# Kernel optimization log

Hardware: AMD Instinct MI355X
Metric: run time of the kernel (lower is better)

## Reference

```python
import jax, jax.numpy as jnp
import numpy as np

T = 0.07  # temperature from init default


def _l2norm(x):
    return x / jnp.linalg.norm(x, axis=1, keepdims=True)


def setup_inputs() -> dict:
    key = jax.random.key(0)
    ks = jax.random.split(key, 12)
    B, D, K = 512, 128, 4096
    G = M = 131072
    return {
        "feat": jax.random.normal(ks[0], (B, D), jnp.float32),
        "label": jax.random.randint(ks[1], (B,), 0, 2),
        "out": jnp.zeros((B, K + 1), jnp.float32),   # unused by forward
        "name": jnp.arange(B),                        # unused by forward
        "y": jax.random.randint(ks[2], (B,), 0, G),   # unused by forward
        "memory_feat_gbm": jax.random.normal(ks[3], (G, D), jnp.float32),
        "memory_prob_gbm": jax.random.uniform(ks[4], (G,), jnp.float32),
        "memory_feat_mate": jax.random.normal(ks[5], (M, D), jnp.float32),
        "memory_prob_mate": jax.random.uniform(ks[6], (M,), jnp.float32),
        "idx_n_g": jax.random.randint(ks[7], (K, 1), 0, G),
        "idx_p_g": jax.random.randint(ks[8], (1, 1), 0, G // 4),
        "idx_n_m": jax.random.randint(ks[9], (K, 1), 0, M),
        "idx_p_m": jax.random.randint(ks[10], (1, 1), 0, M // 4),
    }


def reference(feat, label, out, name, y, memory_feat_gbm, memory_prob_gbm,
              memory_feat_mate, memory_prob_mate, idx_n_g, idx_p_g, idx_n_m, idx_p_m):
    # __init__ normalizes the memory banks once
    mfg = _l2norm(memory_feat_gbm)
    mfm = _l2norm(memory_feat_mate)
    feat_n = _l2norm(feat)  # [B, D]
    output_size = mfg.shape[0]

    # gather positive / negative prototypes (all rows unit-norm, so
    # cosine_similarity == dot product)
    wp_g = mfg[idx_p_g.ravel()]   # [1, D]
    wn_g = mfg[idx_n_g.ravel()]   # [K, D]
    wp_m = mfm[idx_p_m.ravel()]   # [1, D]
    wn_m = mfm[idx_n_m.ravel()]   # [K, D]

    # label==0 (gbm): pos from gbm bank, negs from mate bank; label==1 mirrored
    row_gbm = jnp.concatenate([feat_n @ wp_g.T, feat_n @ wn_m.T], axis=1)   # [B, K+1]
    row_mate = jnp.concatenate([feat_n @ wp_m.T, feat_n @ wn_g.T], axis=1)  # [B, K+1]
    sims = jnp.where((label == 0)[:, None], row_gbm, row_mate)

    # use_softmax=False path: exp(s/T) / Z with Z set from first batch (treated as constant)
    e = jnp.exp(sims / T)
    Z = jax.lax.stop_gradient(e.mean() * output_size)
    out_feature_p_n = e / Z

    # confident cluster members + current batch (data-dependent sizes; eager jax)
    mask_g = memory_prob_gbm > 0.5
    mask_m = memory_prob_mate > 0.6
    feature_clu_all = jnp.concatenate([mfg[mask_g], mfm[mask_m], feat_n], axis=0)
    gt_clu_all = jnp.concatenate([
        jnp.zeros((int(mask_g.sum()),), label.dtype),
        jnp.ones((int(mask_m.sum()),), label.dtype),
        label,
    ], axis=0)
    return out_feature_p_n, feature_clu_all, gt_clu_all
```

## Files before the change

kernel.cpp:

```cpp
#include <hip/hip_runtime.h>
#include <math.h>


#define TINV 14.2857142857142857f
#define JT 64
#define BT 32

__device__ __forceinline__ float wredsum64(float v) {
#pragma unroll
  for (int m = 32; m > 0; m >>= 1) v += __shfl_xor(v, m, 64);
  return v;
}

__global__ __launch_bounds__(256) void k_stageA(
    const float* __restrict__ feat, const int* __restrict__ label,
    const float* __restrict__ mfg, const float* __restrict__ pg,
    const float* __restrict__ mfm, const float* __restrict__ pm,
    const int* __restrict__ idxpg, const int* __restrict__ idxpm,
    float* __restrict__ outp, long long cluTail, long long gtTail,
    int* __restrict__ bucket, int* __restrict__ n0p,
    int* __restrict__ cg, int* __restrict__ cm,
    float* __restrict__ posPartials,
    int B, int K1, int G, int M,
    int nCountBlk, int nFeatBlk, int nPosBlk) {
  int bid = blockIdx.x, t = threadIdx.x;

  if (bid < nCountBlk) {
    __shared__ int s[8];
    int i = bid * 256 + t;
    int a = (i < G) && (pg[i] > 0.5f);
    int b = (i < M) && (pm[i] > 0.6f);
    unsigned long long ba = __ballot(a), bb = __ballot(b);
    int lane = t & 63, w = t >> 6;
    if (lane == 0) { s[w] = __popcll(ba); s[4 + w] = __popcll(bb); }
    __syncthreads();
    if (t == 0) cg[bid] = s[0] + s[1] + s[2] + s[3];
    if (t == 1) cm[bid] = s[4] + s[5] + s[6] + s[7];
    return;
  }
  bid -= nCountBlk;

  if (bid < nFeatBlk) {
    int gid = bid * 256 + t;
    int w = gid >> 6, lane = gid & 63;
    if (w < B) {
      float2 v = ((const float2*)feat)[(long long)w * 64 + lane];
      float sq = wredsum64(v.x * v.x + v.y * v.y);
      float inv = rsqrtf(sq);
      ((float2*)(outp + cluTail))[(long long)w * 64 + lane] =
          make_float2(v.x * inv, v.y * inv);
      if (lane == 0) outp[gtTail + w] = (float)label[w];
    }
    return;
  }
  bid -= nFeatBlk;

  if (bid < nPosBlk) {
    __shared__ float ps[4];
    int gid = bid * 256 + t;
    int w = gid >> 6, lane = gid & 63, lw = t >> 6;
    float e = 0.f;
    if (w < B) {
      int lab = label[w];
      const float* bank = lab ? mfm : mfg;
      long long row = lab ? idxpm[0] : idxpg[0];
      float2 wv = ((const float2*)(bank + row * 128))[lane];
      float2 fv = ((const float2*)feat)[(long long)w * 64 + lane];
      float dot = wredsum64(fv.x * wv.x + fv.y * wv.y);
      float sqw = wredsum64(wv.x * wv.x + wv.y * wv.y);
      float sqf = wredsum64(fv.x * fv.x + fv.y * fv.y);
      e = expf(dot * rsqrtf(sqw) * rsqrtf(sqf) * TINV);
      if (lane == 0) outp[(long long)w * K1] = e;
    }
    if (lane == 0) ps[lw] = e;
    __syncthreads();
    if (t == 0) posPartials[bid] = ps[0] + ps[1] + ps[2] + ps[3];
    return;
  }

  {
    __shared__ int sc[512];
    int t2 = t + 256;
    int m0 = (t < B) ? (label[t] == 0 ? 1 : 0) : 0;
    int m1 = (t2 < B) ? (label[t2] == 0 ? 1 : 0) : 0;
    sc[t] = m0; sc[t2] = m1;
    __syncthreads();
    for (int off = 1; off < 512; off <<= 1) {
      int u0 = (t >= off) ? sc[t - off] : 0;
      int u1 = (t2 >= off) ? sc[t2 - off] : 0;
      __syncthreads();
      sc[t] += u0; sc[t2] += u1;
      __syncthreads();
    }
    int n0 = (B > 0) ? sc[B - 1] : 0;
    if (t < B) {
      int incl = sc[t];
      if (m0) bucket[incl - 1] = t; else bucket[n0 + t - incl] = t;
    }
    if (t2 < B) {
      int incl = sc[t2];
      if (m1) bucket[incl - 1] = t2; else bucket[n0 + t2 - incl] = t2;
    }
    if (t == 0) *n0p = n0;
  }
}

__global__ __launch_bounds__(256) void k_stageB(
    const float* __restrict__ featn, const int* __restrict__ bucket,
    const int* __restrict__ n0ptr,
    const float* __restrict__ mfg, const float* __restrict__ mfm,
    const float* __restrict__ pg, const float* __restrict__ pm,
    const int* __restrict__ idxng, const int* __restrict__ idxnm,
    const int* __restrict__ cg, const int* __restrict__ cm,
    float* __restrict__ out0, float* __restrict__ partials,
    float* __restrict__ outp, long long cluBase, long long gtBase,
    int B, int K, int K1, int G, int M, int NB, int simsGx, int nGatherBlk) {
  int t = threadIdx.x;

  if ((int)blockIdx.x < nGatherBlk) {
    int bid = blockIdx.x;
    int bankId = bid / NB;
    int cb = bid - bankId * NB;
    const float* probs = bankId ? pm : pg;
    const float* rows  = bankId ? mfm : mfg;
    float thr = bankId ? 0.6f : 0.5f;
    int Nelem = bankId ? M : G;
    int lane = t & 63, w = t >> 6;

    int j0 = t, j1 = t + 256;
    int s = 0;
    if (bankId == 0) {
      if (j0 < cb) s += cg[j0];
      if (j1 < cb && j1 < NB) s += cg[j1];
    } else {
      if (j0 < NB) s += cg[j0];
      if (j1 < NB) s += cg[j1];
      if (j0 < cb) s += cm[j0];
      if (j1 < cb && j1 < NB) s += cm[j1];
    }
#pragma unroll
    for (int m = 32; m > 0; m >>= 1) s += __shfl_xor(s, m, 64);

    __shared__ int red[4];
    __shared__ int woff[4];
    __shared__ int selRow[256];
    if (lane == 0) red[w] = s;

    int i = cb * 256 + t;
    int f = (i < Nelem) && (probs[i] > thr);
    unsigned long long mball = __ballot(f);
    if (lane == 0) woff[w] = __popcll(mball);
    __syncthreads();

    long long off = (long long)red[0] + red[1] + red[2] + red[3];
    int pre = 0;
#pragma unroll
    for (int q = 0; q < 3; q++)
      if (q < w) pre += woff[q];
    int S = woff[0] + woff[1] + woff[2] + woff[3];
    unsigned long long below = lane ? ((~0ull) >> (64 - lane)) : 0ull;
    if (f) selRow[pre + __popcll(mball & below)] = i;
    __syncthreads();

    float labv = (float)bankId;
    int hw = t >> 5, l = t & 31;
    for (int r = hw; r < S; r += 8) {
      long long src = selRow[r];
      float4 v = ((const float4*)(rows + src * 128))[l];
      float sq = v.x * v.x + v.y * v.y + v.z * v.z + v.w * v.w;
#pragma unroll
      for (int m = 16; m > 0; m >>= 1) sq += __shfl_xor(sq, m, 64);
      float inv = rsqrtf(sq);
      long long dst = off + r;
      ((float4*)(outp + cluBase + dst * 128))[l] =
          make_float4(v.x * inv, v.y * inv, v.z * inv, v.w * inv);
      if (l == 0) outp[gtBase + dst] = labv;
    }
    return;
  }

  __shared__ float4 wl[JT][33];
  __shared__ float4 fl[BT][33];
  __shared__ float invw[JT];
  __shared__ float bs[4];
  int pidx = (int)blockIdx.x - nGatherBlk;
  int bx = pidx % simsGx, by = pidx / simsGx;
  int n0 = *n0ptr;
  int nb0 = (n0 + BT - 1) / BT;
  int lab, p0, cnt;
  if (by < nb0) {
    lab = 0; p0 = by * BT; cnt = min(BT, n0 - p0);
  } else {
    int k = by - nb0; p0 = n0 + k * BT;
    int n1 = B - n0; cnt = min(BT, n1 - k * BT); lab = 1;
  }
  if (cnt <= 0) { if (t == 0) partials[pidx] = 0.f; return; }
  const float* bank = lab == 0 ? mfm : mfg;
  const int* idxN   = lab == 0 ? idxnm : idxng;
  int j0 = bx * JT;

#pragma unroll
  for (int q = 0; q < 8; q++) {
    int lin = q * 256 + t;
    int row = lin >> 5, col = lin & 31;
    long long srow = idxN[j0 + row];
    wl[row][col] = ((const float4*)(bank + srow * 128))[col];
  }
#pragma unroll
  for (int q = 0; q < 4; q++) {
    int lin = q * 256 + t;
    int row = lin >> 5, col = lin & 31;
    float4 v = make_float4(0.f, 0.f, 0.f, 0.f);
    if (row < cnt) {
      int bg = bucket[p0 + row];
      v = ((const float4*)(featn + (long long)bg * 128))[col];
    }
    fl[row][col] = v;
  }
  __syncthreads();

  {
    int r = t >> 2, q = t & 3;
    float ss = 0.f;
#pragma unroll
    for (int c = 0; c < 8; c++) {
      float4 v = wl[r][q * 8 + c];
      ss += v.x * v.x + v.y * v.y + v.z * v.z + v.w * v.w;
    }
    ss += __shfl_xor(ss, 1, 64);
    ss += __shfl_xor(ss, 2, 64);
    if (q == 0) invw[r] = rsqrtf(ss);
  }
  __syncthreads();

  int tj = t & 15, tb = t >> 4;
  float acc[4][2];
#pragma unroll
  for (int a = 0; a < 4; a++)
#pragma unroll
    for (int b = 0; b < 2; b++) acc[a][b] = 0.f;

#pragma unroll 4
  for (int i = 0; i < 32; i++) {
    float4 w0 = wl[tj][i];
    float4 w1 = wl[tj + 16][i];
    float4 w2 = wl[tj + 32][i];
    float4 w3 = wl[tj + 48][i];
    float4 f0 = fl[tb][i];
    float4 f1 = fl[tb + 16][i];
    acc[0][0] += w0.x*f0.x + w0.y*f0.y + w0.z*f0.z + w0.w*f0.w;
    acc[1][0] += w1.x*f0.x + w1.y*f0.y + w1.z*f0.z + w1.w*f0.w;
    acc[2][0] += w2.x*f0.x + w2.y*f0.y + w2.z*f0.z + w2.w*f0.w;
    acc[3][0] += w3.x*f0.x + w3.y*f0.y + w3.z*f0.z + w3.w*f0.w;
    acc[0][1] += w0.x*f1.x + w0.y*f1.y + w0.z*f1.z + w0.w*f1.w;
    acc[1][1] += w1.x*f1.x + w1.y*f1.y + w1.z*f1.z + w1.w*f1.w;
    acc[2][1] += w2.x*f1.x + w2.y*f1.y + w2.z*f1.z + w2.w*f1.w;
    acc[3][1] += w3.x*f1.x + w3.y*f1.y + w3.z*f1.z + w3.w*f1.w;
  }

  float mysum = 0.f;
#pragma unroll
  for (int bb = 0; bb < 2; bb++) {
    int bl = tb + 16 * bb;
    if (bl < cnt) {
      int bg = bucket[p0 + bl];
#pragma unroll
      for (int jj = 0; jj < 4; jj++) {
        int jr = tj + 16 * jj;
        float e = expf(acc[jj][bb] * invw[jr] * TINV);
        out0[(long long)bg * K1 + 1 + j0 + jr] = e;
        mysum += e;
      }
    }
  }
  float wsum = wredsum64(mysum);
  if ((t & 63) == 0) bs[t >> 6] = wsum;
  __syncthreads();
  if (t == 0) partials[pidx] = bs[0] + bs[1] + bs[2] + bs[3];
}

__global__ __launch_bounds__(256) void k_stageD(
    float* __restrict__ out0, const float* __restrict__ partials, int nPart,
    double factor, long long n4) {
  __shared__ double sd[256];
  int t = threadIdx.x;
  double s = 0.0;
  for (int i = t; i < nPart; i += 256) s += (double)partials[i];
  sd[t] = s;
  __syncthreads();
  for (int off = 128; off > 0; off >>= 1) {
    if (t < off) sd[t] += sd[t + off];
    __syncthreads();
  }
  float sc = (float)(factor / sd[0]);
  long long base = (long long)blockIdx.x * 256 + t;
  long long stride = (long long)gridDim.x * 256;
  for (long long i = base; i < n4; i += stride) {
    float4 v = ((float4*)out0)[i];
    v.x *= sc; v.y *= sc; v.z *= sc; v.w *= sc;
    ((float4*)out0)[i] = v;
  }
}

extern "C" void kernel_launch(void* const* d_in, const int* in_sizes, int n_in,
                              void* d_out, int out_size, void* d_ws,
                              size_t ws_size, hipStream_t stream) {
  const float* feat  = (const float*)d_in[0];
  const int*   label = (const int*)d_in[1];
  const float* mfg   = (const float*)d_in[5];
  const float* pg    = (const float*)d_in[6];
  const float* mfm   = (const float*)d_in[7];
  const float* pm    = (const float*)d_in[8];
  const int*   idxng = (const int*)d_in[9];
  const int*   idxpg = (const int*)d_in[10];
  const int*   idxnm = (const int*)d_in[11];
  const int*   idxpm = (const int*)d_in[12];
  float* outp = (float*)d_out;

  const int B = in_sizes[1];
  const int D = 128;
  const int K = in_sizes[9];
  const int G = in_sizes[6];
  const int M = in_sizes[8];
  const int K1 = K + 1;

  const long long C0 = (long long)B * K1;
  const long long R = ((long long)out_size - C0) / (D + 1);
  const long long G0 = C0 + R * D;
  const long long cluTail = C0 + (R - B) * (long long)D;
  const long long gtTail = G0 + (R - B);

  const float* featn = outp + cluTail;

  char* wsb = (char*)d_ws;
  size_t o = 0;
  auto alloc = [&](size_t bytes) -> char* {
    char* p = wsb + o;
    o = (o + bytes + 255) & ~(size_t)255;
    return p;
  };
  const int simsGx = K / JT;
  const int simsGy = B / BT + 1;
  const int nPartSims = simsGx * simsGy;
  const int nPosBlk = (B * 64 + 255) / 256;
  float* partials = (float*)alloc(sizeof(float) * (nPartSims + nPosBlk));
  int* bucket = (int*)alloc(sizeof(int) * B);
  int* n0p = (int*)alloc(sizeof(int) * 4);
  const int NB = ((G > M ? G : M) + 255) / 256;
  int* cg = (int*)alloc(sizeof(int) * NB);
  int* cm = (int*)alloc(sizeof(int) * NB);
  (void)ws_size; (void)n_in;

  const int nFeatBlk = (B * 64 + 255) / 256;
  const int gridA = NB + nFeatBlk + nPosBlk + 1;
  const int nGatherBlk = 2 * NB;
  const int gridB = nGatherBlk + nPartSims;
  const int gridD = 2048;

  k_stageA<<<gridA, 256, 0, stream>>>(
      feat, label, mfg, pg, mfm, pm, idxpg, idxpm,
      outp, cluTail, gtTail, bucket, n0p, cg, cm,
      partials + nPartSims, B, K1, G, M, NB, nFeatBlk, nPosBlk);

  k_stageB<<<gridB, 256, 0, stream>>>(
      featn, bucket, n0p, mfg, mfm, pg, pm, idxng, idxnm,
      cg, cm, outp, partials, outp, C0, G0,
      B, K, K1, G, M, NB, simsGx, nGatherBlk);

  double factor = (double)B * (double)K1 / (double)G;
  k_stageD<<<gridD, 256, 0, stream>>>(
      outp, partials, nPartSims + nPosBlk, factor, C0 / 4);
}
```

Measured before the change: 52.15 us.

## Refine compaction gather to 64-row chunks and schedule sims blocks first

Stage A now records per-wavefront mask counts in 64-element granularity instead of per 256-element block, which drops a shared-memory barrier. Stage B's gather blocks each handle 64 candidate rows, so there are four times as many blocks but each is shorter. Each half-wave now processes two rows per iteration for more memory-level parallelism, and blocks with no selected rows exit early. The sims tiles are moved to the front of the grid so the heavier GEMM-like blocks start first. In exchange, every gather block scans a prefix array four times longer and more blocks are launched.

```diff
diff --git a/kernel.cpp b/kernel.cpp
--- a/kernel.cpp
+++ b/kernel.cpp
@@ -19,23 +19,22 @@
     const int* __restrict__ idxpg, const int* __restrict__ idxpm,
     float* __restrict__ outp, long long cluTail, long long gtTail,
     int* __restrict__ bucket, int* __restrict__ n0p,
-    int* __restrict__ cg, int* __restrict__ cm,
+    int* __restrict__ cg64, int* __restrict__ cm64,
     float* __restrict__ posPartials,
     int B, int K1, int G, int M,
     int nCountBlk, int nFeatBlk, int nPosBlk) {
   int bid = blockIdx.x, t = threadIdx.x;
 
   if (bid < nCountBlk) {
-    __shared__ int s[8];
     int i = bid * 256 + t;
     int a = (i < G) && (pg[i] > 0.5f);
     int b = (i < M) && (pm[i] > 0.6f);
     unsigned long long ba = __ballot(a), bb = __ballot(b);
     int lane = t & 63, w = t >> 6;
-    if (lane == 0) { s[w] = __popcll(ba); s[4 + w] = __popcll(bb); }
-    __syncthreads();
-    if (t == 0) cg[bid] = s[0] + s[1] + s[2] + s[3];
-    if (t == 1) cm[bid] = s[4] + s[5] + s[6] + s[7];
+    if (lane == 0) {
+      cg64[bid * 4 + w] = __popcll(ba);
+      cm64[bid * 4 + w] = __popcll(bb);
+    }
     return;
   }
   bid -= nCountBlk;
@@ -111,70 +110,77 @@
     const float* __restrict__ mfg, const float* __restrict__ mfm,
     const float* __restrict__ pg, const float* __restrict__ pm,
     const int* __restrict__ idxng, const int* __restrict__ idxnm,
-    const int* __restrict__ cg, const int* __restrict__ cm,
+    const int* __restrict__ cg64, const int* __restrict__ cm64,
     float* __restrict__ out0, float* __restrict__ partials,
     float* __restrict__ outp, long long cluBase, long long gtBase,
-    int B, int K, int K1, int G, int M, int NB, int simsGx, int nGatherBlk) {
+    int B, int K, int K1, int G, int M, int NG64, int simsGx, int nSimsBlk) {
   int t = threadIdx.x;
 
-  if ((int)blockIdx.x < nGatherBlk) {
-    int bid = blockIdx.x;
-    int bankId = bid / NB;
-    int cb = bid - bankId * NB;
+  if ((int)blockIdx.x >= nSimsBlk) {
+    int gb = (int)blockIdx.x - nSimsBlk;
+    int bankId = gb / NG64;
+    int g = gb - bankId * NG64;
     const float* probs = bankId ? pm : pg;
     const float* rows  = bankId ? mfm : mfg;
     float thr = bankId ? 0.6f : 0.5f;
     int Nelem = bankId ? M : G;
     int lane = t & 63, w = t >> 6;
 
-    int j0 = t, j1 = t + 256;
     int s = 0;
-    if (bankId == 0) {
-      if (j0 < cb) s += cg[j0];
-      if (j1 < cb && j1 < NB) s += cg[j1];
-    } else {
-      if (j0 < NB) s += cg[j0];
-      if (j1 < NB) s += cg[j1];
-      if (j0 < cb) s += cm[j0];
-      if (j1 < cb && j1 < NB) s += cm[j1];
+    for (int j = t; j < NG64; j += 256) {
+      if (bankId == 0) {
+        if (j < g) s += cg64[j];
+      } else {
+        s += cg64[j];
+        if (j < g) s += cm64[j];
+      }
     }
 #pragma unroll
     for (int m = 32; m > 0; m >>= 1) s += __shfl_xor(s, m, 64);
 
     __shared__ int red[4];
-    __shared__ int woff[4];
-    __shared__ int selRow[256];
+    __shared__ int selRow[64];
     if (lane == 0) red[w] = s;
 
-    int i = cb * 256 + t;
-    int f = (i < Nelem) && (probs[i] > thr);
-    unsigned long long mball = __ballot(f);
-    if (lane == 0) woff[w] = __popcll(mball);
+    int c = g * 64 + lane;
+    int f = (c < Nelem) && (probs[c] > thr);
+    unsigned long long mb = __ballot(f);
+    if (w == 0) {
+      unsigned long long below = lane ? ((~0ull) >> (64 - lane)) : 0ull;
+      if (f) selRow[__popcll(mb & below)] = c;
+    }
     __syncthreads();
-
+    int S = __popcll(mb);
+    if (S == 0) return;
     long long off = (long long)red[0] + red[1] + red[2] + red[3];
-    int pre = 0;
-#pragma unroll
-    for (int q = 0; q < 3; q++)
-      if (q < w) pre += woff[q];
-    int S = woff[0] + woff[1] + woff[2] + woff[3];
-    unsigned long long below = lane ? ((~0ull) >> (64 - lane)) : 0ull;
-    if (f) selRow[pre + __popcll(mball & below)] = i;
-    __syncthreads();
 
     float labv = (float)bankId;
     int hw = t >> 5, l = t & 31;
-    for (int r = hw; r < S; r += 8) {
-      long long src = selRow[r];
-      float4 v = ((const float4*)(rows + src * 128))[l];
-      float sq = v.x * v.x + v.y * v.y + v.z * v.z + v.w * v.w;
-#pragma unroll
-      for (int m = 16; m > 0; m >>= 1) sq += __shfl_xor(sq, m, 64);
-      float inv = rsqrtf(sq);
-      long long dst = off + r;
-      ((float4*)(outp + cluBase + dst * 128))[l] =
-          make_float4(v.x * inv, v.y * inv, v.z * inv, v.w * inv);
-      if (l == 0) outp[gtBase + dst] = labv;
+    for (int r0 = hw * 2; r0 < S; r0 += 16) {
+      int r1 = r0 + 1;
+      int src0 = selRow[r0];
+      bool has1 = (r1 < S);
+      int src1 = has1 ? selRow[r1] : src0;
+      float4 v0 = ((const float4*)(rows + (long long)src0 * 128))[l];
+      float4 v1 = ((const float4*)(rows + (long long)src1 * 128))[l];
+      float sq0 = v0.x * v0.x + v0.y * v0.y + v0.z * v0.z + v0.w * v0.w;
+      float sq1 = v1.x * v1.x + v1.y * v1.y + v1.z * v1.z + v1.w * v1.w;
+#pragma unroll
+      for (int m = 16; m > 0; m >>= 1) {
+        sq0 += __shfl_xor(sq0, m, 64);
+        sq1 += __shfl_xor(sq1, m, 64);
+      }
+      float i0 = rsqrtf(sq0), i1 = rsqrtf(sq1);
+      long long d0 = off + r0;
+      ((float4*)(outp + cluBase + d0 * 128))[l] =
+          make_float4(v0.x * i0, v0.y * i0, v0.z * i0, v0.w * i0);
+      if (l == 0) outp[gtBase + d0] = labv;
+      if (has1) {
+        long long d1 = off + r1;
+        ((float4*)(outp + cluBase + d1 * 128))[l] =
+            make_float4(v1.x * i1, v1.y * i1, v1.z * i1, v1.w * i1);
+        if (l == 0) outp[gtBase + d1] = labv;
+      }
     }
     return;
   }
@@ -183,7 +189,7 @@
   __shared__ float4 fl[BT][33];
   __shared__ float invw[JT];
   __shared__ float bs[4];
-  int pidx = (int)blockIdx.x - nGatherBlk;
+  int pidx = (int)blockIdx.x;
   int bx = pidx % simsGx, by = pidx / simsGx;
   int n0 = *n0ptr;
   int nb0 = (n0 + BT - 1) / BT;
@@ -347,25 +353,26 @@
   int* bucket = (int*)alloc(sizeof(int) * B);
   int* n0p = (int*)alloc(sizeof(int) * 4);
   const int NB = ((G > M ? G : M) + 255) / 256;
-  int* cg = (int*)alloc(sizeof(int) * NB);
-  int* cm = (int*)alloc(sizeof(int) * NB);
+  const int NG64 = NB * 4;
+  int* cg64 = (int*)alloc(sizeof(int) * NG64);
+  int* cm64 = (int*)alloc(sizeof(int) * NG64);
   (void)ws_size; (void)n_in;
 
   const int nFeatBlk = (B * 64 + 255) / 256;
   const int gridA = NB + nFeatBlk + nPosBlk + 1;
-  const int nGatherBlk = 2 * NB;
-  const int gridB = nGatherBlk + nPartSims;
+  const int nGatherBlk = 2 * NG64;
+  const int gridB = nPartSims + nGatherBlk;
   const int gridD = 2048;
 
   k_stageA<<<gridA, 256, 0, stream>>>(
       feat, label, mfg, pg, mfm, pm, idxpg, idxpm,
-      outp, cluTail, gtTail, bucket, n0p, cg, cm,
+      outp, cluTail, gtTail, bucket, n0p, cg64, cm64,
       partials + nPartSims, B, K1, G, M, NB, nFeatBlk, nPosBlk);
 
   k_stageB<<<gridB, 256, 0, stream>>>(
       featn, bucket, n0p, mfg, mfm, pg, pm, idxng, idxnm,
-      cg, cm, outp, partials, outp, C0, G0,
-      B, K, K1, G, M, NB, simsGx, nGatherBlk);
+      cg64, cm64, outp, partials, outp, C0, G0,
+      B, K, K1, G, M, NG64, simsGx, nPartSims);
 
   double factor = (double)B * (double)K1 / (double)G;
   k_stageD<<<gridD, 256, 0, stream>>>(
```

Result: slower. 59.30 us (+13.7%).

## Move cluster gather from stage B to stage D and batch four rows per iteration

Applied to the files above, without the earlier changes.

The masked cluster-row gather and normalization blocks move out of the similarity kernel and into the final scaling kernel. There they run alongside the scale blocks, whose count drops from 2048 to 1024. The gather loop now handles four rows per half-wave per iteration, so more independent loads are in flight, and it exits early for empty chunks. The aim is to rebalance work across launches and overlap the memory-bound gather with the scaling pass. The trade-off is that each scale block now also repeats the partial-sum reduction, and that pass has fewer blocks.

```diff
diff --git a/kernel.cpp b/kernel.cpp
--- a/kernel.cpp
+++ b/kernel.cpp
@@ -109,81 +109,15 @@
     const float* __restrict__ featn, const int* __restrict__ bucket,
     const int* __restrict__ n0ptr,
     const float* __restrict__ mfg, const float* __restrict__ mfm,
-    const float* __restrict__ pg, const float* __restrict__ pm,
     const int* __restrict__ idxng, const int* __restrict__ idxnm,
-    const int* __restrict__ cg, const int* __restrict__ cm,
     float* __restrict__ out0, float* __restrict__ partials,
-    float* __restrict__ outp, long long cluBase, long long gtBase,
-    int B, int K, int K1, int G, int M, int NB, int simsGx, int nGatherBlk) {
-  int t = threadIdx.x;
-
-  if ((int)blockIdx.x < nGatherBlk) {
-    int bid = blockIdx.x;
-    int bankId = bid / NB;
-    int cb = bid - bankId * NB;
-    const float* probs = bankId ? pm : pg;
-    const float* rows  = bankId ? mfm : mfg;
-    float thr = bankId ? 0.6f : 0.5f;
-    int Nelem = bankId ? M : G;
-    int lane = t & 63, w = t >> 6;
-
-    int j0 = t, j1 = t + 256;
-    int s = 0;
-    if (bankId == 0) {
-      if (j0 < cb) s += cg[j0];
-      if (j1 < cb && j1 < NB) s += cg[j1];
-    } else {
-      if (j0 < NB) s += cg[j0];
-      if (j1 < NB) s += cg[j1];
-      if (j0 < cb) s += cm[j0];
-      if (j1 < cb && j1 < NB) s += cm[j1];
-    }
-#pragma unroll
-    for (int m = 32; m > 0; m >>= 1) s += __shfl_xor(s, m, 64);
-
-    __shared__ int red[4];
-    __shared__ int woff[4];
-    __shared__ int selRow[256];
-    if (lane == 0) red[w] = s;
-
-    int i = cb * 256 + t;
-    int f = (i < Nelem) && (probs[i] > thr);
-    unsigned long long mball = __ballot(f);
-    if (lane == 0) woff[w] = __popcll(mball);
-    __syncthreads();
-
-    long long off = (long long)red[0] + red[1] + red[2] + red[3];
-    int pre = 0;
-#pragma unroll
-    for (int q = 0; q < 3; q++)
-      if (q < w) pre += woff[q];
-    int S = woff[0] + woff[1] + woff[2] + woff[3];
-    unsigned long long below = lane ? ((~0ull) >> (64 - lane)) : 0ull;
-    if (f) selRow[pre + __popcll(mball & below)] = i;
-    __syncthreads();
-
-    float labv = (float)bankId;
-    int hw = t >> 5, l = t & 31;
-    for (int r = hw; r < S; r += 8) {
-      long long src = selRow[r];
-      float4 v = ((const float4*)(rows + src * 128))[l];
-      float sq = v.x * v.x + v.y * v.y + v.z * v.z + v.w * v.w;
-#pragma unroll
-      for (int m = 16; m > 0; m >>= 1) sq += __shfl_xor(sq, m, 64);
-      float inv = rsqrtf(sq);
-      long long dst = off + r;
-      ((float4*)(outp + cluBase + dst * 128))[l] =
-          make_float4(v.x * inv, v.y * inv, v.z * inv, v.w * inv);
-      if (l == 0) outp[gtBase + dst] = labv;
-    }
-    return;
-  }
-
+    int B, int K, int K1, int simsGx) {
   __shared__ float4 wl[JT][33];
   __shared__ float4 fl[BT][33];
   __shared__ float invw[JT];
   __shared__ float bs[4];
-  int pidx = (int)blockIdx.x - nGatherBlk;
+  int t = threadIdx.x;
+  int pidx = (int)blockIdx.x;
   int bx = pidx % simsGx, by = pidx / simsGx;
   int n0 = *n0ptr;
   int nb0 = (n0 + BT - 1) / BT;
@@ -280,10 +214,111 @@
 }
 
 __global__ __launch_bounds__(256) void k_stageD(
+    const float* __restrict__ mfg, const float* __restrict__ mfm,
+    const float* __restrict__ pg, const float* __restrict__ pm,
+    const int* __restrict__ cg, const int* __restrict__ cm,
+    float* __restrict__ outp, long long cluBase, long long gtBase,
+    int G, int M, int NB, int nGatherBlk,
     float* __restrict__ out0, const float* __restrict__ partials, int nPart,
     double factor, long long n4) {
+  int t = threadIdx.x;
+
+  if ((int)blockIdx.x < nGatherBlk) {
+    __shared__ int red[4];
+    __shared__ int woff[4];
+    __shared__ int selRow[256];
+    int bid = blockIdx.x;
+    int bankId = bid / NB;
+    int cb = bid - bankId * NB;
+    const float* probs = bankId ? pm : pg;
+    const float* rows  = bankId ? mfm : mfg;
+    float thr = bankId ? 0.6f : 0.5f;
+    int Nelem = bankId ? M : G;
+    int lane = t & 63, w = t >> 6;
+
+    int j0 = t, j1 = t + 256;
+    int s = 0;
+    if (bankId == 0) {
+      if (j0 < cb) s += cg[j0];
+      if (j1 < cb && j1 < NB) s += cg[j1];
+    } else {
+      if (j0 < NB) s += cg[j0];
+      if (j1 < NB) s += cg[j1];
+      if (j0 < cb) s += cm[j0];
+      if (j1 < cb && j1 < NB) s += cm[j1];
+    }
+#pragma unroll
+    for (int m = 32; m > 0; m >>= 1) s += __shfl_xor(s, m, 64);
+    if (lane == 0) red[w] = s;
+
+    int i = cb * 256 + t;
+    int f = (i < Nelem) && (probs[i] > thr);
+    unsigned long long mb = __ballot(f);
+    if (lane == 0) woff[w] = __popcll(mb);
+    __syncthreads();
+
+    long long off = (long long)red[0] + red[1] + red[2] + red[3];
+    int pre = 0;
+#pragma unroll
+    for (int q = 0; q < 3; q++)
+      if (q < w) pre += woff[q];
+    int S = woff[0] + woff[1] + woff[2] + woff[3];
+    unsigned long long below = lane ? ((~0ull) >> (64 - lane)) : 0ull;
+    if (f) selRow[pre + __popcll(mb & below)] = i;
+    __syncthreads();
+    if (S == 0) return;
+
+    float labv = (float)bankId;
+    int hw = t >> 5, l = t & 31;
+    for (int r0 = hw * 4; r0 < S; r0 += 32) {
+      int r1 = r0 + 1, r2 = r0 + 2, r3 = r0 + 3;
+      int s0 = selRow[r0];
+      int s1 = selRow[r1 < S ? r1 : r0];
+      int s2 = selRow[r2 < S ? r2 : r0];
+      int s3 = selRow[r3 < S ? r3 : r0];
+      float4 v0 = ((const float4*)(rows + (long long)s0 * 128))[l];
+      float4 v1 = ((const float4*)(rows + (long long)s1 * 128))[l];
+      float4 v2 = ((const float4*)(rows + (long long)s2 * 128))[l];
+      float4 v3 = ((const float4*)(rows + (long long)s3 * 128))[l];
+      float q0 = v0.x*v0.x + v0.y*v0.y + v0.z*v0.z + v0.w*v0.w;
+      float q1 = v1.x*v1.x + v1.y*v1.y + v1.z*v1.z + v1.w*v1.w;
+      float q2 = v2.x*v2.x + v2.y*v2.y + v2.z*v2.z + v2.w*v2.w;
+      float q3 = v3.x*v3.x + v3.y*v3.y + v3.z*v3.z + v3.w*v3.w;
+#pragma unroll
+      for (int m = 16; m > 0; m >>= 1) {
+        q0 += __shfl_xor(q0, m, 64);
+        q1 += __shfl_xor(q1, m, 64);
+        q2 += __shfl_xor(q2, m, 64);
+        q3 += __shfl_xor(q3, m, 64);
+      }
+      float i0 = rsqrtf(q0), i1 = rsqrtf(q1), i2 = rsqrtf(q2), i3 = rsqrtf(q3);
+      long long d0 = off + r0;
+      ((float4*)(outp + cluBase + d0 * 128))[l] =
+          make_float4(v0.x*i0, v0.y*i0, v0.z*i0, v0.w*i0);
+      if (l == 0) outp[gtBase + d0] = labv;
+      if (r1 < S) {
+        long long d = off + r1;
+        ((float4*)(outp + cluBase + d * 128))[l] =
+            make_float4(v1.x*i1, v1.y*i1, v1.z*i1, v1.w*i1);
+        if (l == 0) outp[gtBase + d] = labv;
+      }
+      if (r2 < S) {
+        long long d = off + r2;
+        ((float4*)(outp + cluBase + d * 128))[l] =
+            make_float4(v2.x*i2, v2.y*i2, v2.z*i2, v2.w*i2);
+        if (l == 0) outp[gtBase + d] = labv;
+      }
+      if (r3 < S) {
+        long long d = off + r3;
+        ((float4*)(outp + cluBase + d * 128))[l] =
+            make_float4(v3.x*i3, v3.y*i3, v3.z*i3, v3.w*i3);
+        if (l == 0) outp[gtBase + d] = labv;
+      }
+    }
+    return;
+  }
+
   __shared__ double sd[256];
-  int t = threadIdx.x;
   double s = 0.0;
   for (int i = t; i < nPart; i += 256) s += (double)partials[i];
   sd[t] = s;
@@ -293,8 +328,8 @@
     __syncthreads();
   }
   float sc = (float)(factor / sd[0]);
-  long long base = (long long)blockIdx.x * 256 + t;
-  long long stride = (long long)gridDim.x * 256;
+  long long base = (long long)((int)blockIdx.x - nGatherBlk) * 256 + t;
+  long long stride = (long long)(gridDim.x - nGatherBlk) * 256;
   for (long long i = base; i < n4; i += stride) {
     float4 v = ((float4*)out0)[i];
     v.x *= sc; v.y *= sc; v.z *= sc; v.w *= sc;
@@ -353,9 +388,10 @@
 
   const int nFeatBlk = (B * 64 + 255) / 256;
   const int gridA = NB + nFeatBlk + nPosBlk + 1;
+  const int gridB = nPartSims;
   const int nGatherBlk = 2 * NB;
-  const int gridB = nGatherBlk + nPartSims;
-  const int gridD = 2048;
+  const int nScaleBlk = 1024;
+  const int gridD = nGatherBlk + nScaleBlk;
 
   k_stageA<<<gridA, 256, 0, stream>>>(
       feat, label, mfg, pg, mfm, pm, idxpg, idxpm,
@@ -363,11 +399,11 @@
       partials + nPartSims, B, K1, G, M, NB, nFeatBlk, nPosBlk);
 
   k_stageB<<<gridB, 256, 0, stream>>>(
-      featn, bucket, n0p, mfg, mfm, pg, pm, idxng, idxnm,
-      cg, cm, outp, partials, outp, C0, G0,
-      B, K, K1, G, M, NB, simsGx, nGatherBlk);
+      featn, bucket, n0p, mfg, mfm, idxng, idxnm,
+      outp, partials, B, K, K1, simsGx);
 
   double factor = (double)B * (double)K1 / (double)G;
   k_stageD<<<gridD, 256, 0, stream>>>(
+      mfg, mfm, pg, pm, cg, cm, outp, C0, G0, G, M, NB, nGatherBlk,
       outp, partials, nPartSims + nPosBlk, factor, C0 / 4);
 }
```

Measured after the change: 53.67 us. +2.9%, slower.
